# Optimization experiments

Measured on AMD Instinct MI355X. Metric: run time of the kernel, lower is better.

## Reference

```python
import jax, jax.numpy as jnp
import numpy as np
from jax import lax

B, L, H, KSIZE = 8, 16384, 128, 65
PAD = KSIZE // 2  # 32; odd kernel keeps output length == L


def setup_inputs() -> dict:
    key = jax.random.key(0)
    kq, kk, kv, kw = jax.random.split(key, 4)
    Q = jax.random.normal(kq, (B, L, H), dtype=jnp.float32)
    K = jax.random.normal(kk, (B, L, H), dtype=jnp.float32)
    V = jax.random.normal(kv, (B, L, H), dtype=jnp.float32)
    # Conv1d weight [out_ch, in_ch, kernel], kaiming-like scale
    W = jax.random.normal(kw, (H, H, KSIZE), dtype=jnp.float32) / np.sqrt(H * KSIZE)
    return {"Q": Q, "K": K, "V": V, "W": W}


def reference(Q, K, V, W):
    # [B, L, H] -> [B, H, L] (channels-first, matching torch transpose(1,2))
    Qt = jnp.swapaxes(Q, 1, 2)
    Kt = jnp.swapaxes(K, 1, 2)
    Vt = jnp.swapaxes(V, 1, 2)
    # Conv1d over sequence dim; lax conv is cross-correlation like torch
    conv_q = lax.conv_general_dilated(
        Qt, W,
        window_strides=(1,),
        padding=[(PAD, PAD)],
        dimension_numbers=("NCH", "OIH", "NCH"),
    )  # [B, H, L]
    scores = conv_q * Kt                      # elementwise gate
    A = jax.nn.softmax(scores, axis=-1)       # softmax over sequence dim
    Z = A * Vt                                # weighted V (elementwise)
    return jnp.swapaxes(Z, 1, 2)              # back to [B, L, H]
```

## Files before the change

kernel.cpp:

```cpp
#include <hip/hip_runtime.h>
#include <stdint.h>

#define BATCH 8
#define LSEQ 16384
#define HDIM 128
#define KSZ 65
#define PADW 32
#define LH (LSEQ*HDIM)
#define TL 256
#define NROWS (TL + 2*PADW)
#define LBLKS (LSEQ/TL)
#define EXP_SHIFT 20.0f

#define WS_WBF_OFF 4096

typedef __attribute__((ext_vector_type(8))) short bf16x8;
typedef __attribute__((ext_vector_type(4))) short bf16x4;
typedef __attribute__((ext_vector_type(16))) float f32x16;

__device__ __forceinline__ unsigned short f2bf(float f) {
  unsigned int u = __float_as_uint(f);
  return (unsigned short)((u + 0x7FFFu + ((u >> 16) & 1u)) >> 16);
}

__global__ __launch_bounds__(256) void wcvt_kernel(const float* __restrict__ W,
                                                   unsigned short* __restrict__ Wbf) {
  __shared__ float lw[KSZ*HDIM];
  const int o = blockIdx.x;
  const float* src = W + (size_t)o * (HDIM*KSZ);
  for (int t = threadIdx.x; t < HDIM*KSZ; t += 256) lw[t] = src[t];
  __syncthreads();
  const int osw = (o & 15) << 3;
  for (int idx = threadIdx.x; idx < KSZ*HDIM; idx += 256) {
    const int k = idx >> 7;
    const int i = idx & 127;
    Wbf[(size_t)k*(HDIM*HDIM) + o*HDIM + (i ^ osw)] = f2bf(lw[i*KSZ + k]);
  }
}

__device__ __forceinline__ void stage_w(const unsigned short* __restrict__ Wbf, int k,
                                        unsigned short* dst, int w, int lane) {
  const char* gbase = (const char*)(Wbf + (size_t)k * (HDIM*HDIM));
  char* lbase = (char*)dst;
#pragma unroll
  for (int r = 0; r < 4; ++r) {
    const int off = r*8192 + w*1024;
    __builtin_amdgcn_global_load_lds(
        (const __attribute__((address_space(1))) unsigned int*)(gbase + off + lane*16),
        (__attribute__((address_space(3))) unsigned int*)(lbase + off),
        16, 0, 0);
  }
}

__global__ __launch_bounds__(512, 2) void conv_gate_kernel(
    const float* __restrict__ Qm, const float* __restrict__ Km,
    const unsigned short* __restrict__ Wbf,
    float* __restrict__ Eout, float* __restrict__ gsum) {

  __shared__ __align__(16) unsigned short Qs[NROWS*HDIM];
  __shared__ __align__(16) unsigned short Ws[2][HDIM*HDIM];

  const int tid  = threadIdx.x;
  const int lane = tid & 63;
  const int w    = tid >> 6;
  const int wr   = w >> 1;
  const int wc   = w & 1;
  const int l31  = lane & 31;
  const int hi2  = lane >> 5;

  const int bx = blockIdx.x;
  const int b  = bx >> 6;
  const int l0 = (bx & 63) << 8;

  {
    const int r0 = tid >> 5;
    const int c4 = (tid & 31) << 2;
    const float* qbase = Qm + (size_t)b*LH + c4;
#pragma unroll
    for (int it = 0; it < NROWS/16; ++it) {
      const int r = it*16 + r0;
      const int grow = l0 - PADW + r;
      bf16x4 pk = {0, 0, 0, 0};
      if (grow >= 0 && grow < LSEQ) {
        const float4 qv = *(const float4*)(qbase + (size_t)grow*HDIM);
        pk[0] = (short)f2bf(qv.x); pk[1] = (short)f2bf(qv.y);
        pk[2] = (short)f2bf(qv.z); pk[3] = (short)f2bf(qv.w);
      }
      *(bf16x4*)(&Qs[r*HDIM + (c4 ^ ((r & 15) << 3))]) = pk;
    }
  }

  stage_w(Wbf, 0, &Ws[0][0], w, lane);

  int bofs[2][8];
#pragma unroll
  for (int nf = 0; nf < 2; ++nf) {
    const int o  = wc*64 + nf*32 + l31;
    const int xr = (o & 15) << 3;
#pragma unroll
    for (int kk = 0; kk < 8; ++kk)
      bofs[nf][kk] = o*HDIM + ((kk*16 + hi2*8) ^ xr);
  }

  f32x16 acc[2][2] = {};

  __syncthreads();

  const int arow0 = wr*64 + l31;
  int buf = 0;
  for (int k = 0; k < KSZ; ++k) {
    if (k < KSZ-1) stage_w(Wbf, k+1, &Ws[buf^1][0], w, lane);
    const unsigned short* wsrc = &Ws[buf][0];
    const int rb = k + arow0;
    const int r0 = rb, r1 = rb + 32;
    const int xa0 = (r0 & 15) << 3, xa1 = (r1 & 15) << 3;

    bf16x8 aC[2], bC[2], aN[2], bN[2];
    {
      const int i0 = hi2*8;
      aC[0] = *(const bf16x8*)(&Qs[r0*HDIM + (i0 ^ xa0)]);
      aC[1] = *(const bf16x8*)(&Qs[r1*HDIM + (i0 ^ xa1)]);
      bC[0] = *(const bf16x8*)(&wsrc[bofs[0][0]]);
      bC[1] = *(const bf16x8*)(&wsrc[bofs[1][0]]);
    }
#pragma unroll
    for (int kk = 0; kk < 8; ++kk) {
      if (kk < 7) {
        const int i0 = (kk+1)*16 + hi2*8;
        aN[0] = *(const bf16x8*)(&Qs[r0*HDIM + (i0 ^ xa0)]);
        aN[1] = *(const bf16x8*)(&Qs[r1*HDIM + (i0 ^ xa1)]);
        bN[0] = *(const bf16x8*)(&wsrc[bofs[0][kk+1]]);
        bN[1] = *(const bf16x8*)(&wsrc[bofs[1][kk+1]]);
      }
      __builtin_amdgcn_s_setprio(1);
      acc[0][0] = __builtin_amdgcn_mfma_f32_32x32x16_bf16(aC[0], bC[0], acc[0][0], 0, 0, 0);
      acc[0][1] = __builtin_amdgcn_mfma_f32_32x32x16_bf16(aC[0], bC[1], acc[0][1], 0, 0, 0);
      acc[1][0] = __builtin_amdgcn_mfma_f32_32x32x16_bf16(aC[1], bC[0], acc[1][0], 0, 0, 0);
      acc[1][1] = __builtin_amdgcn_mfma_f32_32x32x16_bf16(aC[1], bC[1], acc[1][1], 0, 0, 0);
      __builtin_amdgcn_s_setprio(0);
      aC[0] = aN[0]; aC[1] = aN[1]; bC[0] = bN[0]; bC[1] = bN[1];
    }
    __syncthreads();
    buf ^= 1;
  }

  float psum[2] = {0.f, 0.f};
#pragma unroll
  for (int mf = 0; mf < 2; ++mf) {
#pragma unroll
    for (int r = 0; r < 16; ++r) {
      const int row = wr*64 + mf*32 + (r & 3) + 8*(r >> 2) + 4*hi2;
      const size_t gb = (size_t)b*LH + (size_t)(l0 + row)*HDIM + wc*64 + l31;
#pragma unroll
      for (int nf = 0; nf < 2; ++nf) {
        const float s = acc[mf][nf][r] * Km[gb + nf*32];
        const float e = __expf(s - EXP_SHIFT);
        Eout[gb + nf*32] = e;
        psum[nf] += e;
      }
    }
  }
  psum[0] += __shfl_xor(psum[0], 32);
  psum[1] += __shfl_xor(psum[1], 32);
  if (hi2 == 0) {
    atomicAdd(&gsum[b*HDIM + wc*64 + l31],      psum[0]);
    atomicAdd(&gsum[b*HDIM + wc*64 + 32 + l31], psum[1]);
  }
}

__global__ __launch_bounds__(256) void finalize_kernel(float* __restrict__ out,
                                                       const float* __restrict__ V,
                                                       const float* __restrict__ gsum) {
  const int total4 = (BATCH*LH) >> 2;
  const int stride = gridDim.x * blockDim.x;
  for (int f = blockIdx.x*blockDim.x + threadIdx.x; f < total4; f += stride) {
    const float4 e = ((const float4*)out)[f];
    const float4 v = ((const float4*)V)[f];
    const int e0 = f << 2;
    const float* gs = gsum + ((e0 >> 21) << 7) + (e0 & 127);
    float4 z;
    z.x = e.x * v.x / gs[0];
    z.y = e.y * v.y / gs[1];
    z.z = e.z * v.z / gs[2];
    z.w = e.w * v.w / gs[3];
    ((float4*)out)[f] = z;
  }
}

extern "C" void kernel_launch(void* const* d_in, const int* in_sizes, int n_in,
                              void* d_out, int out_size, void* d_ws, size_t ws_size,
                              hipStream_t stream) {
  (void)in_sizes; (void)n_in; (void)out_size; (void)ws_size;
  const float* Q = (const float*)d_in[0];
  const float* K = (const float*)d_in[1];
  const float* V = (const float*)d_in[2];
  const float* W = (const float*)d_in[3];
  float* out  = (float*)d_out;
  float* gsum = (float*)d_ws;
  unsigned short* Wbf = (unsigned short*)((char*)d_ws + WS_WBF_OFF);

  hipMemsetAsync(d_ws, 0, BATCH*HDIM*sizeof(float), stream);
  wcvt_kernel<<<HDIM, 256, 0, stream>>>(W, Wbf);
  conv_gate_kernel<<<BATCH*LBLKS, 512, 0, stream>>>(Q, K, Wbf, out, gsum);
  finalize_kernel<<<2048, 256, 0, stream>>>(out, V, gsum);
}
```

Baseline: 297.2 us.

## Load conv weights as pre-swizzled MFMA fragments directly from global memory

The weight-conversion kernel now writes the bf16 weights in MFMA B-fragment order, so each lane reads its 16-byte operand straight from global memory. This removes the double-buffered LDS staging of weights and the per-tap block barrier. The smaller LDS footprint lets the launch bound target four blocks per CU instead of two. In exchange, every wave issues its own global/L2 loads for the weights, and the manual register prefetch of the next fragment is gone, so latency hiding now relies on occupancy.

After: 335.4 us. +12.8%, slower.

```diff
diff --git a/kernel.cpp b/kernel.cpp
--- a/kernel.cpp
+++ b/kernel.cpp
@@ -30,35 +30,25 @@
   const float* src = W + (size_t)o * (HDIM*KSZ);
   for (int t = threadIdx.x; t < HDIM*KSZ; t += 256) lw[t] = src[t];
   __syncthreads();
-  const int osw = (o & 15) << 3;
+  const int ob  = o >> 5;
+  const int l31 = o & 31;
   for (int idx = threadIdx.x; idx < KSZ*HDIM; idx += 256) {
     const int k = idx >> 7;
     const int i = idx & 127;
-    Wbf[(size_t)k*(HDIM*HDIM) + o*HDIM + (i ^ osw)] = f2bf(lw[i*KSZ + k]);
+    const int kk  = i >> 4;
+    const int hi2 = (i >> 3) & 1;
+    const int e   = i & 7;
+    const size_t dst = ((((size_t)(k*4 + ob)*8 + kk)*2 + hi2)*32 + l31)*8 + e;
+    Wbf[dst] = f2bf(lw[i*KSZ + k]);
   }
 }
 
-__device__ __forceinline__ void stage_w(const unsigned short* __restrict__ Wbf, int k,
-                                        unsigned short* dst, int w, int lane) {
-  const char* gbase = (const char*)(Wbf + (size_t)k * (HDIM*HDIM));
-  char* lbase = (char*)dst;
-#pragma unroll
-  for (int r = 0; r < 4; ++r) {
-    const int off = r*8192 + w*1024;
-    __builtin_amdgcn_global_load_lds(
-        (const __attribute__((address_space(1))) unsigned int*)(gbase + off + lane*16),
-        (__attribute__((address_space(3))) unsigned int*)(lbase + off),
-        16, 0, 0);
-  }
-}
-
-__global__ __launch_bounds__(512, 2) void conv_gate_kernel(
+__global__ __launch_bounds__(512, 4) void conv_gate_kernel(
     const float* __restrict__ Qm, const float* __restrict__ Km,
-    const unsigned short* __restrict__ Wbf,
+    const unsigned short* __restrict__ Wfrag,
     float* __restrict__ Eout, float* __restrict__ gsum) {
 
   __shared__ __align__(16) unsigned short Qs[NROWS*HDIM];
-  __shared__ __align__(16) unsigned short Ws[2][HDIM*HDIM];
 
   const int tid  = threadIdx.x;
   const int lane = tid & 63;
@@ -90,58 +80,32 @@
     }
   }
 
-  stage_w(Wbf, 0, &Ws[0][0], w, lane);
-
-  int bofs[2][8];
-#pragma unroll
-  for (int nf = 0; nf < 2; ++nf) {
-    const int o  = wc*64 + nf*32 + l31;
-    const int xr = (o & 15) << 3;
-#pragma unroll
-    for (int kk = 0; kk < 8; ++kk)
-      bofs[nf][kk] = o*HDIM + ((kk*16 + hi2*8) ^ xr);
-  }
+  const unsigned short* pb = Wfrag + (size_t)(wc*2)*4096 + hi2*256 + l31*8;
 
   f32x16 acc[2][2] = {};
 
   __syncthreads();
 
   const int arow0 = wr*64 + l31;
-  int buf = 0;
   for (int k = 0; k < KSZ; ++k) {
-    if (k < KSZ-1) stage_w(Wbf, k+1, &Ws[buf^1][0], w, lane);
-    const unsigned short* wsrc = &Ws[buf][0];
-    const int rb = k + arow0;
-    const int r0 = rb, r1 = rb + 32;
+    const unsigned short* pk = pb + (size_t)k*16384;
+    const int r0 = k + arow0;
+    const int r1 = r0 + 32;
     const int xa0 = (r0 & 15) << 3, xa1 = (r1 & 15) << 3;
-
-    bf16x8 aC[2], bC[2], aN[2], bN[2];
-    {
-      const int i0 = hi2*8;
-      aC[0] = *(const bf16x8*)(&Qs[r0*HDIM + (i0 ^ xa0)]);
-      aC[1] = *(const bf16x8*)(&Qs[r1*HDIM + (i0 ^ xa1)]);
-      bC[0] = *(const bf16x8*)(&wsrc[bofs[0][0]]);
-      bC[1] = *(const bf16x8*)(&wsrc[bofs[1][0]]);
-    }
 #pragma unroll
     for (int kk = 0; kk < 8; ++kk) {
-      if (kk < 7) {
-        const int i0 = (kk+1)*16 + hi2*8;
-        aN[0] = *(const bf16x8*)(&Qs[r0*HDIM + (i0 ^ xa0)]);
-        aN[1] = *(const bf16x8*)(&Qs[r1*HDIM + (i0 ^ xa1)]);
-        bN[0] = *(const bf16x8*)(&wsrc[bofs[0][kk+1]]);
-        bN[1] = *(const bf16x8*)(&wsrc[bofs[1][kk+1]]);
-      }
+      const int i0 = kk*16 + hi2*8;
+      const bf16x8 a0 = *(const bf16x8*)(&Qs[r0*HDIM + (i0 ^ xa0)]);
+      const bf16x8 a1 = *(const bf16x8*)(&Qs[r1*HDIM + (i0 ^ xa1)]);
+      const bf16x8 b0 = *(const bf16x8*)(pk + kk*512);
+      const bf16x8 b1 = *(const bf16x8*)(pk + 4096 + kk*512);
       __builtin_amdgcn_s_setprio(1);
-      acc[0][0] = __builtin_amdgcn_mfma_f32_32x32x16_bf16(aC[0], bC[0], acc[0][0], 0, 0, 0);
-      acc[0][1] = __builtin_amdgcn_mfma_f32_32x32x16_bf16(aC[0], bC[1], acc[0][1], 0, 0, 0);
-      acc[1][0] = __builtin_amdgcn_mfma_f32_32x32x16_bf16(aC[1], bC[0], acc[1][0], 0, 0, 0);
-      acc[1][1] = __builtin_amdgcn_mfma_f32_32x32x16_bf16(aC[1], bC[1], acc[1][1], 0, 0, 0);
+      acc[0][0] = __builtin_amdgcn_mfma_f32_32x32x16_bf16(a0, b0, acc[0][0], 0, 0, 0);
+      acc[0][1] = __builtin_amdgcn_mfma_f32_32x32x16_bf16(a0, b1, acc[0][1], 0, 0, 0);
+      acc[1][0] = __builtin_amdgcn_mfma_f32_32x32x16_bf16(a1, b0, acc[1][0], 0, 0, 0);
+      acc[1][1] = __builtin_amdgcn_mfma_f32_32x32x16_bf16(a1, b1, acc[1][1], 0, 0, 0);
       __builtin_amdgcn_s_setprio(0);
-      aC[0] = aN[0]; aC[1] = aN[1]; bC[0] = bN[0]; bC[1] = bN[1];
     }
-    __syncthreads();
-    buf ^= 1;
   }
 
   float psum[2] = {0.f, 0.f};
```
